# Performance work log

Hardware: AMD Instinct MI355X
Metric: run time of the kernel (lower is better)

The kernel has to match this reference:

```python
import jax, jax.numpy as jnp
import numpy as np
from jax import lax

B, L, D_MODEL = 2, 2048, 768
D_STATE, D_INNER, DT_RANK, K = 16, 1536, 48, 4


def setup_inputs() -> dict:
    key = jax.random.key(0)
    ks = jax.random.split(key, 10)
    x = jax.random.normal(ks[0], (B, L, D_MODEL), dtype=jnp.float32)
    in_proj_w = 0.02 * jax.random.normal(ks[1], (2 * D_INNER, D_MODEL), dtype=jnp.float32)
    conv_w = 0.1 * jax.random.normal(ks[2], (D_INNER, 1, K), dtype=jnp.float32)
    conv_b = 0.01 * jax.random.normal(ks[3], (D_INNER,), dtype=jnp.float32)
    # A_log initialized as log(1..d_state) per channel (as in _init_parameters)
    A_log = jnp.tile(jnp.log(jnp.arange(1, D_STATE + 1, dtype=jnp.float32)), (D_INNER, 1))
    D_param = jnp.ones((D_INNER,), dtype=jnp.float32)
    x_proj_w = 0.02 * jax.random.normal(ks[4], (DT_RANK + 2 * D_STATE, D_INNER), dtype=jnp.float32)
    dt_proj_w = jax.random.uniform(ks[5], (D_INNER, DT_RANK), minval=-0.1, maxval=0.1, dtype=jnp.float32)
    dt_proj_b = 0.01 * jax.random.normal(ks[6], (D_INNER,), dtype=jnp.float32)
    out_proj_w = 0.02 * jax.random.normal(ks[7], (D_MODEL, D_INNER), dtype=jnp.float32)
    return {"x": x, "in_proj_w": in_proj_w, "conv_w": conv_w, "conv_b": conv_b,
            "A_log": A_log, "D_param": D_param, "x_proj_w": x_proj_w,
            "dt_proj_w": dt_proj_w, "dt_proj_b": dt_proj_b, "out_proj_w": out_proj_w}


def _forward(x, in_proj_w, conv_w, conv_b, A_log, D_param, x_proj_w, dt_proj_w, dt_proj_b, out_proj_w):
    xz = jnp.einsum('bld,ed->ble', x, in_proj_w)            # [B,L,2*d_inner]
    xp, z = jnp.split(xz, 2, axis=-1)                        # [B,L,d_inner] each
    # depthwise causal conv1d: torch Conv1d(padding=3)[..., :L] == left-pad 3, valid conv
    xc = lax.conv_general_dilated(
        xp.transpose(0, 2, 1), conv_w, window_strides=(1,),
        padding=[(K - 1, 0)], feature_group_count=D_INNER)   # [B,d_inner,L]
    xc = (xc + conv_b[None, :, None]).transpose(0, 2, 1)     # [B,L,d_inner]
    xc = jax.nn.silu(xc)
    x_dbl = jnp.einsum('bld,ed->ble', xc, x_proj_w)          # [B,L,dt_rank+2*d_state]
    dt_low, Bmat, Cmat = jnp.split(x_dbl, [DT_RANK, DT_RANK + D_STATE], axis=-1)
    dt = jax.nn.softplus(jnp.einsum('blr,dr->bld', dt_low, dt_proj_w) + dt_proj_b)  # [B,L,d_inner]
    A = -jnp.exp(A_log)                                      # [d_inner,d_state]
    A_bar = jnp.exp(dt[..., None] * A[None, None])           # [B,L,d_inner,d_state]
    Bx = (dt * xc)[..., None] * Bmat[:, :, None, :]          # [B,L,d_inner,d_state]
    # time-major scan over the recurrence h = A_bar*h + B_bar*x
    A_t = A_bar.transpose(1, 0, 2, 3)
    Bx_t = Bx.transpose(1, 0, 2, 3)
    C_t = Cmat.transpose(1, 0, 2)                            # [L,B,d_state]
    h0 = jnp.zeros((B, D_INNER, D_STATE), dtype=x.dtype)

    def step(h, inp):
        a, bx, c = inp
        h = a * h + bx
        y = jnp.einsum('bds,bs->bd', h, c)
        return h, y

    _, ys = lax.scan(step, h0, (A_t, Bx_t, C_t))             # ys: [L,B,d_inner]
    y = ys.transpose(1, 0, 2)
    y = y + xc * D_param
    y = y * jax.nn.silu(z)
    return jnp.einsum('bld,md->blm', y, out_proj_w)          # [B,L,d_model]


def reference(x, in_proj_w, conv_w, conv_b, A_log, D_param, x_proj_w, dt_proj_w, dt_proj_b, out_proj_w):
    return _forward(x, in_proj_w, conv_w, conv_b, A_log, D_param, x_proj_w, dt_proj_w, dt_proj_b, out_proj_w)
```

## Files before the change

kernel.cpp:

```cpp
#include <hip/hip_runtime.h>
#include <stdint.h>

#define B_SZ    2
#define L_SEQ   2048
#define DMODEL  768
#define DSTATE  16
#define DINNER  1536
#define DTRANK  48
#define M_ROWS  4096
#define NCHUNK  32
#define TCHUNK  64
#define PADL    68

typedef __attribute__((ext_vector_type(8))) short bf16x8;
typedef __attribute__((ext_vector_type(4))) float f32x4;
typedef __attribute__((ext_vector_type(4))) unsigned int u32x4;

__device__ __forceinline__ unsigned short f2bf(float f) {
  unsigned int u = __float_as_uint(f);
  u += 0x7FFFu + ((u >> 16) & 1u);
  return (unsigned short)(u >> 16);
}
__device__ __forceinline__ float bf2f(unsigned short h) {
  return __uint_as_float(((unsigned int)h) << 16);
}
__device__ __forceinline__ float fexp(float x) {
  return __builtin_amdgcn_exp2f(x * 1.44269504088896340736f);
}
__device__ __forceinline__ float sigm(float x) {
  return 1.0f / (1.0f + fexp(-x));
}

template <int CTRL>
__device__ __forceinline__ float dpp_add(float v) {
  int x = __builtin_amdgcn_update_dpp(0, __float_as_int(v), CTRL, 0xF, 0xF, true);
  return v + __int_as_float(x);
}
__device__ __forceinline__ float row16_sum(float v) {
  v = dpp_add<0xB1>(v);
  v = dpp_add<0x4E>(v);
  v = dpp_add<0x124>(v);
  v = dpp_add<0x128>(v);
  return v;
}

__global__ void cast_all_kernel(const float* __restrict__ x, const float* __restrict__ w1,
                                const float* __restrict__ w2, const float* __restrict__ w3,
                                const float* __restrict__ dtw,
                                unsigned short* __restrict__ xbf, unsigned short* __restrict__ w1bf,
                                unsigned short* __restrict__ w2bf, unsigned short* __restrict__ w3bf,
                                unsigned short* __restrict__ dtwbf) {
  int i = blockIdx.x * 256 + threadIdx.x;
  const int n_x = M_ROWS * DMODEL;
  const int n_w1 = 2 * DINNER * DMODEL;
  const int n_w3 = DMODEL * DINNER;
  const int n_w2 = 128 * DINNER;
  const int n_dtw = DINNER * 64;
  if (i < n_x)  { xbf[i] = f2bf(x[i]); return; }  i -= n_x;
  if (i < n_w1) { w1bf[i] = f2bf(w1[i]); return; } i -= n_w1;
  if (i < n_w3) { w3bf[i] = f2bf(w3[i]); return; } i -= n_w3;
  if (i < n_w2) {
    int row = i / DINNER, col = i - row * DINNER;
    w2bf[i] = (row < (DTRANK + 2 * DSTATE)) ? f2bf(w2[row * DINNER + col]) : (unsigned short)0;
    return;
  }
  i -= n_w2;
  if (i < n_dtw) {
    int row = i >> 6, col = i & 63;
    dtwbf[i] = (col < DTRANK) ? f2bf(dtw[row * DTRANK + col]) : (unsigned short)0;
  }
}

__global__ void cast_dtlow_kernel(const float* __restrict__ xdbl, unsigned short* __restrict__ out) {
  int i = blockIdx.x * 256 + threadIdx.x;
  int row = i >> 6, col = i & 63;
  out[i] = (col < DTRANK) ? f2bf(xdbl[row * 128 + col]) : (unsigned short)0;
}

template <int EPI>
__global__ __launch_bounds__(256, 2) void gemm_bt(
    const unsigned short* __restrict__ A, const unsigned short* __restrict__ Bt,
    float* __restrict__ C, int K, int ldc, const float* __restrict__ bias) {
  __shared__ unsigned short As[128 * 40];
  __shared__ unsigned short Bs[128 * 40];
  const int tid = threadIdx.x;
  const int m0 = blockIdx.x * 128;
  const int n0 = blockIdx.y * 128;
  const int lane = tid & 63;
  const int wave = tid >> 6;
  const int wr = (wave >> 1) * 64, wc = (wave & 1) * 64;
  const int lm = lane & 15, q = lane >> 4;
  const int r = tid >> 2, sg = (tid & 3) * 8;

  f32x4 acc[4][4] = {};

  for (int k0 = 0; k0 < K; k0 += 32) {
    u32x4 a0 = *(const u32x4*)(A + (size_t)(m0 + r) * K + k0 + sg);
    u32x4 a1 = *(const u32x4*)(A + (size_t)(m0 + r + 64) * K + k0 + sg);
    u32x4 b0 = *(const u32x4*)(Bt + (size_t)(n0 + r) * K + k0 + sg);
    u32x4 b1 = *(const u32x4*)(Bt + (size_t)(n0 + r + 64) * K + k0 + sg);
    __syncthreads();
    *(u32x4*)&As[r * 40 + sg] = a0;
    *(u32x4*)&As[(r + 64) * 40 + sg] = a1;
    *(u32x4*)&Bs[r * 40 + sg] = b0;
    *(u32x4*)&Bs[(r + 64) * 40 + sg] = b1;
    __syncthreads();
    bf16x8 af[4], bq[4];
#pragma unroll
    for (int mt = 0; mt < 4; mt++)
      af[mt] = *(const bf16x8*)&As[(wr + mt * 16 + lm) * 40 + q * 8];
#pragma unroll
    for (int nt = 0; nt < 4; nt++)
      bq[nt] = *(const bf16x8*)&Bs[(wc + nt * 16 + lm) * 40 + q * 8];
#pragma unroll
    for (int mt = 0; mt < 4; mt++)
#pragma unroll
      for (int nt = 0; nt < 4; nt++)
        acc[mt][nt] = __builtin_amdgcn_mfma_f32_16x16x32_bf16(af[mt], bq[nt], acc[mt][nt], 0, 0, 0);
  }

#pragma unroll
  for (int mt = 0; mt < 4; mt++) {
    int row0 = m0 + wr + mt * 16 + q * 4;
#pragma unroll
    for (int nt = 0; nt < 4; nt++) {
      int col = n0 + wc + nt * 16 + lm;
      float bs = 0.f;
      if (EPI == 1) bs = bias[col];
#pragma unroll
      for (int i = 0; i < 4; i++) {
        float v = acc[mt][nt][i];
        if (EPI == 1) {
          v += bs;
          v = (v > 15.f) ? v : log1pf(fexp(v));
        }
        C[(size_t)(row0 + i) * ldc + col] = v;
      }
    }
  }
}

__global__ void conv_silu_kernel(const float* __restrict__ xz, const float* __restrict__ cw,
                                 const float* __restrict__ cb, unsigned short* __restrict__ xcbf) {
  int idx = blockIdx.x * 256 + threadIdx.x;
  if (idx >= B_SZ * L_SEQ * DINNER) return;
  int d = idx % DINNER;
  int bl = idx / DINNER;
  int l = bl & (L_SEQ - 1);
  float acc = cb[d];
#pragma unroll
  for (int k = 0; k < 4; k++) {
    int ll = l - 3 + k;
    if (ll >= 0) acc += cw[d * 4 + k] * xz[(size_t)(bl - 3 + k) * 3072 + d];
  }
  xcbf[idx] = f2bf(acc * sigm(acc));
}

__global__ __launch_bounds__(256) void scan_phase1(
    const float* __restrict__ dt, const unsigned short* __restrict__ xcbf,
    const float* __restrict__ xdbl, const float* __restrict__ A_log,
    float* __restrict__ P, float* __restrict__ HL) {
  __shared__ float dts[16 * PADL], xcs[16 * PADL], Bsh[16 * PADL];
  const int tid = threadIdx.x;
  const int db = blockIdx.x * 16;
  const int b = blockIdx.y;
  const int c = blockIdx.z;
  const int l0c = c * TCHUNK;
  {
    const int di = tid & 15, lg = tid >> 4;
    f32x4 dv, xv, bv;
#pragma unroll
    for (int j = 0; j < 4; j++) {
      size_t row = (size_t)(b * L_SEQ + l0c + lg * 4 + j);
      dv[j] = dt[row * DINNER + db + di];
      xv[j] = bf2f(xcbf[row * DINNER + db + di]);
      bv[j] = xdbl[row * 128 + DTRANK + di];
    }
    *(f32x4*)&dts[di * PADL + lg * 4] = dv;
    *(f32x4*)&xcs[di * PADL + lg * 4] = xv;
    *(f32x4*)&Bsh[di * PADL + lg * 4] = bv;
  }
  __syncthreads();
  const int s = tid & 15, dl = tid >> 4;
  const int d = db + dl;
  const float a2 = -fexp(A_log[d * 16 + s]) * 1.44269504f;
  float h = 0.f, sdt = 0.f;
  for (int l0 = 0; l0 < TCHUNK; l0 += 4) {
    f32x4 dtv = *(const f32x4*)&dts[dl * PADL + l0];
    f32x4 xcv = *(const f32x4*)&xcs[dl * PADL + l0];
    f32x4 Bv  = *(const f32x4*)&Bsh[s * PADL + l0];
#pragma unroll
    for (int j = 0; j < 4; j++) {
      float a = __builtin_amdgcn_exp2f(dtv[j] * a2);
      h = a * h + dtv[j] * xcv[j] * Bv[j];
      sdt += dtv[j];
    }
  }
  size_t o = ((size_t)(c * B_SZ + b) * DINNER + d) * 16 + s;
  P[o] = __builtin_amdgcn_exp2f(a2 * sdt);
  HL[o] = h;
}

__global__ void scan_phase2(const float* __restrict__ P, const float* __restrict__ HL,
                            float* __restrict__ HIN) {
  int tg = blockIdx.x * 256 + threadIdx.x;
  int s = tg & 15;
  int rem = tg >> 4;
  int d = rem % DINNER;
  int b = rem / DINNER;
  float h = 0.f;
  for (int c = 0; c < NCHUNK; c++) {
    size_t o = ((size_t)(c * B_SZ + b) * DINNER + d) * 16 + s;
    HIN[o] = h;
    h = P[o] * h + HL[o];
  }
}

__global__ __launch_bounds__(256) void scan_phase3(
    const float* __restrict__ dt, const unsigned short* __restrict__ xcbf,
    const float* __restrict__ xdbl, const float* __restrict__ A_log,
    const float* __restrict__ HIN, const float* __restrict__ xz,
    const float* __restrict__ Dp, unsigned short* __restrict__ ybf) {
  __shared__ float dts[16 * PADL], xcs[16 * PADL], Bsh[16 * PADL], Csh[16 * PADL], ysh[16 * PADL];
  const int tid = threadIdx.x;
  const int db = blockIdx.x * 16;
  const int b = blockIdx.y;
  const int c = blockIdx.z;
  const int l0c = c * TCHUNK;
  const int di = tid & 15, lg = tid >> 4;
  {
    f32x4 dv, xv, bv, cv;
#pragma unroll
    for (int j = 0; j < 4; j++) {
      size_t row = (size_t)(b * L_SEQ + l0c + lg * 4 + j);
      dv[j] = dt[row * DINNER + db + di];
      xv[j] = bf2f(xcbf[row * DINNER + db + di]);
      bv[j] = xdbl[row * 128 + DTRANK + di];
      cv[j] = xdbl[row * 128 + DTRANK + DSTATE + di];
    }
    *(f32x4*)&dts[di * PADL + lg * 4] = dv;
    *(f32x4*)&xcs[di * PADL + lg * 4] = xv;
    *(f32x4*)&Bsh[di * PADL + lg * 4] = bv;
    *(f32x4*)&Csh[di * PADL + lg * 4] = cv;
  }
  __syncthreads();
  const int s = tid & 15, dl = tid >> 4;
  const int d = db + dl;
  const float a2 = -fexp(A_log[d * 16 + s]) * 1.44269504f;
  float h = HIN[((size_t)(c * B_SZ + b) * DINNER + d) * 16 + s];
  for (int l0 = 0; l0 < TCHUNK; l0 += 4) {
    f32x4 dtv = *(const f32x4*)&dts[dl * PADL + l0];
    f32x4 xcv = *(const f32x4*)&xcs[dl * PADL + l0];
    f32x4 Bv  = *(const f32x4*)&Bsh[s * PADL + l0];
    f32x4 Cv  = *(const f32x4*)&Csh[s * PADL + l0];
    f32x4 y4;
#pragma unroll
    for (int j = 0; j < 4; j++) {
      float a = __builtin_amdgcn_exp2f(dtv[j] * a2);
      h = a * h + dtv[j] * xcv[j] * Bv[j];
      y4[j] = row16_sum(h * Cv[j]);
    }
    if (s == 0) *(f32x4*)&ysh[dl * PADL + l0] = y4;
  }
  __syncthreads();
#pragma unroll
  for (int i = 0; i < 4; i++) {
    int l = lg + i * 16;
    size_t row = (size_t)(b * L_SEQ + l0c + l);
    int gd = db + di;
    float zv = xz[row * 3072 + DINNER + gd];
    float yv = ysh[di * PADL + l] + xcs[di * PADL + l] * Dp[gd];
    ybf[row * DINNER + gd] = f2bf(yv * zv * sigm(zv));
  }
}

extern "C" void kernel_launch(void* const* d_in, const int* in_sizes, int n_in,
                              void* d_out, int out_size, void* d_ws, size_t ws_size,
                              hipStream_t stream) {
  const float* x    = (const float*)d_in[0];
  const float* w1   = (const float*)d_in[1];
  const float* cw   = (const float*)d_in[2];
  const float* cb   = (const float*)d_in[3];
  const float* alog = (const float*)d_in[4];
  const float* Dp   = (const float*)d_in[5];
  const float* w2   = (const float*)d_in[6];
  const float* dtw  = (const float*)d_in[7];
  const float* dtb  = (const float*)d_in[8];
  const float* w3   = (const float*)d_in[9];
  float* out = (float*)d_out;
  char* ws = (char*)d_ws;

  size_t off = 0;
  auto alloc = [&](size_t bytes) { size_t o = off; off += (bytes + 255) & ~(size_t)255; return o; };
  float*          xz    = (float*)(ws + alloc((size_t)M_ROWS * 3072 * 4));
  float*          xdbl  = (float*)(ws + alloc((size_t)M_ROWS * 128 * 4));
  float*          dtf   = (float*)(ws + alloc((size_t)M_ROWS * DINNER * 4));
  unsigned short* xbf   = (unsigned short*)(ws + alloc((size_t)M_ROWS * DMODEL * 2));
  unsigned short* w1bf  = (unsigned short*)(ws + alloc((size_t)2 * DINNER * DMODEL * 2));
  unsigned short* w2bf  = (unsigned short*)(ws + alloc((size_t)128 * DINNER * 2));
  unsigned short* w3bf  = (unsigned short*)(ws + alloc((size_t)DMODEL * DINNER * 2));
  unsigned short* dtlbf = (unsigned short*)(ws + alloc((size_t)M_ROWS * 64 * 2));
  unsigned short* dtwbf = (unsigned short*)(ws + alloc((size_t)DINNER * 64 * 2));
  unsigned short* xcbf  = (unsigned short*)(ws + alloc((size_t)M_ROWS * DINNER * 2));
  unsigned short* ybf   = (unsigned short*)(ws + alloc((size_t)M_ROWS * DINNER * 2));
  float*          Pbuf  = (float*)(ws + alloc((size_t)NCHUNK * B_SZ * DINNER * 16 * 4));
  float*          HLbuf = (float*)(ws + alloc((size_t)NCHUNK * B_SZ * DINNER * 16 * 4));
  float*          HINb  = (float*)(ws + alloc((size_t)NCHUNK * B_SZ * DINNER * 16 * 4));

  cast_all_kernel<<<27264, 256, 0, stream>>>(x, w1, w2, w3, dtw, xbf, w1bf, w2bf, w3bf, dtwbf);
  gemm_bt<0><<<dim3(32, 24), 256, 0, stream>>>(xbf, w1bf, xz, DMODEL, 3072, nullptr);
  conv_silu_kernel<<<24576, 256, 0, stream>>>(xz, cw, cb, xcbf);
  gemm_bt<0><<<dim3(32, 1), 256, 0, stream>>>(xcbf, w2bf, xdbl, DINNER, 128, nullptr);
  cast_dtlow_kernel<<<1024, 256, 0, stream>>>(xdbl, dtlbf);
  gemm_bt<1><<<dim3(32, 12), 256, 0, stream>>>(dtlbf, dtwbf, dtf, 64, DINNER, dtb);
  scan_phase1<<<dim3(96, 2, 32), 256, 0, stream>>>(dtf, xcbf, xdbl, alog, Pbuf, HLbuf);
  scan_phase2<<<192, 256, 0, stream>>>(Pbuf, HLbuf, HINb);
  scan_phase3<<<dim3(96, 2, 32), 256, 0, stream>>>(dtf, xcbf, xdbl, alog, HINb, xz, Dp, ybf);
  gemm_bt<0><<<dim3(32, 6), 256, 0, stream>>>(ybf, w3bf, out, DINNER, 768, nullptr);
}
```

Baseline: 337.3 us.

## Replace chunked three-phase scan with single-pass scan over transposed channel-major inputs

```diff
diff --git a/kernel.cpp b/kernel.cpp
--- a/kernel.cpp
+++ b/kernel.cpp
@@ -9,12 +9,11 @@
 #define DTRANK  48
 #define M_ROWS  4096
 #define NCHUNK  32
-#define TCHUNK  64
-#define PADL    68
 
 typedef __attribute__((ext_vector_type(8))) short bf16x8;
 typedef __attribute__((ext_vector_type(4))) float f32x4;
 typedef __attribute__((ext_vector_type(4))) unsigned int u32x4;
+typedef __attribute__((ext_vector_type(2))) unsigned int u32x2;
 
 __device__ __forceinline__ unsigned short f2bf(float f) {
   unsigned int u = __float_as_uint(f);
@@ -36,11 +35,9 @@
   int x = __builtin_amdgcn_update_dpp(0, __float_as_int(v), CTRL, 0xF, 0xF, true);
   return v + __int_as_float(x);
 }
-__device__ __forceinline__ float row16_sum(float v) {
+__device__ __forceinline__ float quad_sum(float v) {
   v = dpp_add<0xB1>(v);
   v = dpp_add<0x4E>(v);
-  v = dpp_add<0x124>(v);
-  v = dpp_add<0x128>(v);
   return v;
 }
 
@@ -122,16 +119,19 @@
 #pragma unroll
   for (int mt = 0; mt < 4; mt++) {
     int row0 = m0 + wr + mt * 16 + q * 4;
+    float bs4[4];
+    if (EPI == 2) {
+#pragma unroll
+      for (int i = 0; i < 4; i++) bs4[i] = bias[row0 + i];
+    }
 #pragma unroll
     for (int nt = 0; nt < 4; nt++) {
       int col = n0 + wc + nt * 16 + lm;
-      float bs = 0.f;
-      if (EPI == 1) bs = bias[col];
 #pragma unroll
       for (int i = 0; i < 4; i++) {
         float v = acc[mt][nt][i];
-        if (EPI == 1) {
-          v += bs;
+        if (EPI == 2) {
+          v += bs4[i];
           v = (v > 15.f) ? v : log1pf(fexp(v));
         }
         C[(size_t)(row0 + i) * ldc + col] = v;
@@ -156,121 +156,173 @@
   xcbf[idx] = f2bf(acc * sigm(acc));
 }
 
-__global__ __launch_bounds__(256) void scan_phase1(
-    const float* __restrict__ dt, const unsigned short* __restrict__ xcbf,
-    const float* __restrict__ xdbl, const float* __restrict__ A_log,
-    float* __restrict__ P, float* __restrict__ HL) {
-  __shared__ float dts[16 * PADL], xcs[16 * PADL], Bsh[16 * PADL];
+__global__ __launch_bounds__(256) void transpose_bf16(const unsigned short* __restrict__ in,
+                                                      unsigned short* __restrict__ out) {
+  __shared__ unsigned short tl[64 * 80];
+  const int r0 = blockIdx.x * 64;
+  const int c0 = blockIdx.y * 64;
   const int tid = threadIdx.x;
-  const int db = blockIdx.x * 16;
+#pragma unroll
+  for (int it = 0; it < 2; it++) {
+    int idx = tid + it * 256;
+    int rr = idx >> 3, cs = idx & 7;
+    u32x4 v = *(const u32x4*)(in + (size_t)(r0 + rr) * DINNER + c0 + cs * 8);
+    *(u32x4*)&tl[rr * 80 + cs * 8] = v;
+  }
+  __syncthreads();
+#pragma unroll
+  for (int it = 0; it < 2; it++) {
+    int idx = tid + it * 256;
+    int cc = idx & 63, rs = idx >> 6;
+    rs += it * 0;
+    rs = (tid + it * 256) >> 6;
+    unsigned int w[4];
+#pragma unroll
+    for (int p = 0; p < 4; p++) {
+      unsigned int lo = tl[(rs * 8 + 2 * p) * 80 + cc];
+      unsigned int hi = tl[(rs * 8 + 2 * p + 1) * 80 + cc];
+      w[p] = lo | (hi << 16);
+    }
+    *(u32x4*)(out + (size_t)(c0 + cc) * M_ROWS + r0 + rs * 8) = *(u32x4*)w;
+  }
+}
+
+__global__ __launch_bounds__(256) void transpose_silu(const float* __restrict__ xz,
+                                                      unsigned short* __restrict__ out) {
+  __shared__ float tl[64 * 68];
+  const int r0 = blockIdx.x * 64;
+  const int c0 = blockIdx.y * 64;
+  const int tid = threadIdx.x;
+#pragma unroll
+  for (int it = 0; it < 4; it++) {
+    int idx = tid + it * 256;
+    int rr = idx >> 4, cs = idx & 15;
+    f32x4 v = *(const f32x4*)(xz + (size_t)(r0 + rr) * 3072 + DINNER + c0 + cs * 4);
+#pragma unroll
+    for (int p = 0; p < 4; p++) v[p] = v[p] * sigm(v[p]);
+    *(f32x4*)&tl[rr * 68 + cs * 4] = v;
+  }
+  __syncthreads();
+#pragma unroll
+  for (int it = 0; it < 2; it++) {
+    int idx = tid + it * 256;
+    int cc = idx & 63, rs = idx >> 6;
+    unsigned int w[4];
+#pragma unroll
+    for (int p = 0; p < 4; p++) {
+      unsigned int lo = f2bf(tl[(rs * 8 + 2 * p) * 68 + cc]);
+      unsigned int hi = f2bf(tl[(rs * 8 + 2 * p + 1) * 68 + cc]);
+      w[p] = lo | (hi << 16);
+    }
+    *(u32x4*)(out + (size_t)(c0 + cc) * M_ROWS + r0 + rs * 8) = *(u32x4*)w;
+  }
+}
+
+__global__ void bct_kernel(const float* __restrict__ xdbl, float* __restrict__ BCt) {
+  int t = blockIdx.x * 256 + threadIdx.x;
+  int l4 = t & 511;
+  int j  = (t >> 9) & 31;
+  int b  = (t >> 14) & 1;
+  f32x4 o;
+#pragma unroll
+  for (int i = 0; i < 4; i++)
+    o[i] = xdbl[((size_t)b * L_SEQ + l4 * 4 + i) * 128 + DTRANK + j];
+  *(f32x4*)(BCt + ((size_t)b * 32 + j) * L_SEQ + l4 * 4) = o;
+}
+
+__global__ __launch_bounds__(64) void scan_single(
+    const float* __restrict__ dtT, const unsigned short* __restrict__ xcT,
+    const float* __restrict__ BCt, const unsigned short* __restrict__ szT,
+    const float* __restrict__ A_log, const float* __restrict__ Dp,
+    unsigned short* __restrict__ ybf) {
+  __shared__ float ysh[16 * 68];
+  const int lane = threadIdx.x;
+  const int s = lane & 15, dl = lane >> 4;
+  const int d = blockIdx.x * 4 + dl;
   const int b = blockIdx.y;
-  const int c = blockIdx.z;
-  const int l0c = c * TCHUNK;
-  {
-    const int di = tid & 15, lg = tid >> 4;
-    f32x4 dv, xv, bv;
-#pragma unroll
-    for (int j = 0; j < 4; j++) {
-      size_t row = (size_t)(b * L_SEQ + l0c + lg * 4 + j);
-      dv[j] = dt[row * DINNER + db + di];
-      xv[j] = bf2f(xcbf[row * DINNER + db + di]);
-      bv[j] = xdbl[row * 128 + DTRANK + di];
-    }
-    *(f32x4*)&dts[di * PADL + lg * 4] = dv;
-    *(f32x4*)&xcs[di * PADL + lg * 4] = xv;
-    *(f32x4*)&Bsh[di * PADL + lg * 4] = bv;
-  }
-  __syncthreads();
-  const int s = tid & 15, dl = tid >> 4;
-  const int d = db + dl;
+  const size_t rbase = (size_t)b * L_SEQ;
   const float a2 = -fexp(A_log[d * 16 + s]) * 1.44269504f;
-  float h = 0.f, sdt = 0.f;
-  for (int l0 = 0; l0 < TCHUNK; l0 += 4) {
-    f32x4 dtv = *(const f32x4*)&dts[dl * PADL + l0];
-    f32x4 xcv = *(const f32x4*)&xcs[dl * PADL + l0];
-    f32x4 Bv  = *(const f32x4*)&Bsh[s * PADL + l0];
-#pragma unroll
-    for (int j = 0; j < 4; j++) {
-      float a = __builtin_amdgcn_exp2f(dtv[j] * a2);
-      h = a * h + dtv[j] * xcv[j] * Bv[j];
-      sdt += dtv[j];
-    }
-  }
-  size_t o = ((size_t)(c * B_SZ + b) * DINNER + d) * 16 + s;
-  P[o] = __builtin_amdgcn_exp2f(a2 * sdt);
-  HL[o] = h;
-}
-
-__global__ void scan_phase2(const float* __restrict__ P, const float* __restrict__ HL,
-                            float* __restrict__ HIN) {
-  int tg = blockIdx.x * 256 + threadIdx.x;
-  int s = tg & 15;
-  int rem = tg >> 4;
-  int d = rem % DINNER;
-  int b = rem / DINNER;
+  const float dpv = Dp[d];
+  const float* dtrow = dtT + (size_t)d * M_ROWS + rbase;
+  const unsigned short* xcrow = xcT + (size_t)d * M_ROWS + rbase;
+  const unsigned short* szrow = szT + (size_t)d * M_ROWS + rbase;
+  const float* Brow = BCt + ((size_t)b * 32 + s) * L_SEQ;
+  const float* Crow = BCt + ((size_t)b * 32 + 16 + s) * L_SEQ;
+  float* ywp = &ysh[(dl * 4 + (s >> 2)) * 68 + (s & 3)];
+  const bool sb0 = (s & 1) != 0, sb1 = (s & 2) != 0;
   float h = 0.f;
+
+  f32x4 ndt0 = *(const f32x4*)(dtrow);
+  f32x4 ndt1 = *(const f32x4*)(dtrow + 4);
+  u32x4 nxc  = *(const u32x4*)(xcrow);
+  f32x4 nB0  = *(const f32x4*)(Brow);
+  f32x4 nB1  = *(const f32x4*)(Brow + 4);
+  f32x4 nC0  = *(const f32x4*)(Crow);
+  f32x4 nC1  = *(const f32x4*)(Crow + 4);
+
   for (int c = 0; c < NCHUNK; c++) {
-    size_t o = ((size_t)(c * B_SZ + b) * DINNER + d) * 16 + s;
-    HIN[o] = h;
-    h = P[o] * h + HL[o];
-  }
-}
-
-__global__ __launch_bounds__(256) void scan_phase3(
-    const float* __restrict__ dt, const unsigned short* __restrict__ xcbf,
-    const float* __restrict__ xdbl, const float* __restrict__ A_log,
-    const float* __restrict__ HIN, const float* __restrict__ xz,
-    const float* __restrict__ Dp, unsigned short* __restrict__ ybf) {
-  __shared__ float dts[16 * PADL], xcs[16 * PADL], Bsh[16 * PADL], Csh[16 * PADL], ysh[16 * PADL];
-  const int tid = threadIdx.x;
-  const int db = blockIdx.x * 16;
-  const int b = blockIdx.y;
-  const int c = blockIdx.z;
-  const int l0c = c * TCHUNK;
-  const int di = tid & 15, lg = tid >> 4;
-  {
-    f32x4 dv, xv, bv, cv;
-#pragma unroll
-    for (int j = 0; j < 4; j++) {
-      size_t row = (size_t)(b * L_SEQ + l0c + lg * 4 + j);
-      dv[j] = dt[row * DINNER + db + di];
-      xv[j] = bf2f(xcbf[row * DINNER + db + di]);
-      bv[j] = xdbl[row * 128 + DTRANK + di];
-      cv[j] = xdbl[row * 128 + DTRANK + DSTATE + di];
-    }
-    *(f32x4*)&dts[di * PADL + lg * 4] = dv;
-    *(f32x4*)&xcs[di * PADL + lg * 4] = xv;
-    *(f32x4*)&Bsh[di * PADL + lg * 4] = bv;
-    *(f32x4*)&Csh[di * PADL + lg * 4] = cv;
-  }
-  __syncthreads();
-  const int s = tid & 15, dl = tid >> 4;
-  const int d = db + dl;
-  const float a2 = -fexp(A_log[d * 16 + s]) * 1.44269504f;
-  float h = HIN[((size_t)(c * B_SZ + b) * DINNER + d) * 16 + s];
-  for (int l0 = 0; l0 < TCHUNK; l0 += 4) {
-    f32x4 dtv = *(const f32x4*)&dts[dl * PADL + l0];
-    f32x4 xcv = *(const f32x4*)&xcs[dl * PADL + l0];
-    f32x4 Bv  = *(const f32x4*)&Bsh[s * PADL + l0];
-    f32x4 Cv  = *(const f32x4*)&Csh[s * PADL + l0];
-    f32x4 y4;
-#pragma unroll
-    for (int j = 0; j < 4; j++) {
-      float a = __builtin_amdgcn_exp2f(dtv[j] * a2);
-      h = a * h + dtv[j] * xcv[j] * Bv[j];
-      y4[j] = row16_sum(h * Cv[j]);
-    }
-    if (s == 0) *(f32x4*)&ysh[dl * PADL + l0] = y4;
-  }
-  __syncthreads();
-#pragma unroll
-  for (int i = 0; i < 4; i++) {
-    int l = lg + i * 16;
-    size_t row = (size_t)(b * L_SEQ + l0c + l);
-    int gd = db + di;
-    float zv = xz[row * 3072 + DINNER + gd];
-    float yv = ysh[di * PADL + l] + xcs[di * PADL + l] * Dp[gd];
-    ybf[row * DINNER + gd] = f2bf(yv * zv * sigm(zv));
+#pragma unroll 1
+    for (int g = 0; g < 8; g++) {
+      f32x4 dt0 = ndt0, dt1 = ndt1, B0 = nB0, B1 = nB1, C0 = nC0, C1 = nC1;
+      u32x4 xcv = nxc;
+      int ln = c * 64 + g * 8 + 8;
+      if (ln == L_SEQ) ln = 0;
+      ndt0 = *(const f32x4*)(dtrow + ln);
+      ndt1 = *(const f32x4*)(dtrow + ln + 4);
+      nxc  = *(const u32x4*)(xcrow + ln);
+      nB0  = *(const f32x4*)(Brow + ln);
+      nB1  = *(const f32x4*)(Brow + ln + 4);
+      nC0  = *(const f32x4*)(Crow + ln);
+      nC1  = *(const f32x4*)(Crow + ln + 4);
+
+      float xf[8];
+#pragma unroll
+      for (int jp = 0; jp < 4; jp++) {
+        unsigned int w = xcv[jp];
+        xf[2 * jp]     = __uint_as_float(w << 16);
+        xf[2 * jp + 1] = __uint_as_float(w & 0xFFFF0000u);
+      }
+      float p[8];
+#pragma unroll
+      for (int j = 0; j < 8; j++) {
+        float dtj = (j < 4) ? dt0[j] : dt1[j - 4];
+        float Bj  = (j < 4) ? B0[j]  : B1[j - 4];
+        float Cj  = (j < 4) ? C0[j]  : C1[j - 4];
+        float a = __builtin_amdgcn_exp2f(dtj * a2);
+        h = a * h + dtj * xf[j] * Bj;
+        p[j] = h * Cj;
+      }
+#pragma unroll
+      for (int half = 0; half < 2; half++) {
+        float q0 = quad_sum(p[half * 4 + 0]);
+        float q1 = quad_sum(p[half * 4 + 1]);
+        float q2 = quad_sum(p[half * 4 + 2]);
+        float q3 = quad_sum(p[half * 4 + 3]);
+        float v01 = sb0 ? q1 : q0;
+        float v23 = sb0 ? q3 : q2;
+        ywp[g * 8 + half * 4] = sb1 ? v23 : v01;
+      }
+    }
+    {
+      f32x4 y0 = *(const f32x4*)&ysh[(dl * 4 + 0) * 68 + s * 4];
+      f32x4 y1 = *(const f32x4*)&ysh[(dl * 4 + 1) * 68 + s * 4];
+      f32x4 y2 = *(const f32x4*)&ysh[(dl * 4 + 2) * 68 + s * 4];
+      f32x4 y3 = *(const f32x4*)&ysh[(dl * 4 + 3) * 68 + s * 4];
+      f32x4 ys = y0 + y1 + y2 + y3;
+      const int le = c * 64 + s * 4;
+      u32x2 xcu = *(const u32x2*)(xcrow + le);
+      u32x2 szu = *(const u32x2*)(szrow + le);
+      float xcf[4] = {__uint_as_float(xcu[0] << 16), __uint_as_float(xcu[0] & 0xFFFF0000u),
+                      __uint_as_float(xcu[1] << 16), __uint_as_float(xcu[1] & 0xFFFF0000u)};
+      float szf[4] = {__uint_as_float(szu[0] << 16), __uint_as_float(szu[0] & 0xFFFF0000u),
+                      __uint_as_float(szu[1] << 16), __uint_as_float(szu[1] & 0xFFFF0000u)};
+      size_t rr0 = rbase + le;
+#pragma unroll
+      for (int i = 0; i < 4; i++) {
+        float yv = ys[i] + xcf[i] * dpv;
+        ybf[(rr0 + i) * DINNER + d] = f2bf(yv * szf[i]);
+      }
+    }
   }
 }
 
@@ -292,9 +344,11 @@
 
   size_t off = 0;
   auto alloc = [&](size_t bytes) { size_t o = off; off += (bytes + 255) & ~(size_t)255; return o; };
-  float*          xz    = (float*)(ws + alloc((size_t)M_ROWS * 3072 * 4));
+  char*           xzr   = ws + alloc((size_t)M_ROWS * 3072 * 4);
+  float*          xz    = (float*)xzr;
+  float*          dtT   = (float*)xzr;
+  unsigned short* ybf   = (unsigned short*)(xzr + (size_t)DINNER * M_ROWS * 4);
   float*          xdbl  = (float*)(ws + alloc((size_t)M_ROWS * 128 * 4));
-  float*          dtf   = (float*)(ws + alloc((size_t)M_ROWS * DINNER * 4));
   unsigned short* xbf   = (unsigned short*)(ws + alloc((size_t)M_ROWS * DMODEL * 2));
   unsigned short* w1bf  = (unsigned short*)(ws + alloc((size_t)2 * DINNER * DMODEL * 2));
   unsigned short* w2bf  = (unsigned short*)(ws + alloc((size_t)128 * DINNER * 2));
@@ -302,19 +356,19 @@
   unsigned short* dtlbf = (unsigned short*)(ws + alloc((size_t)M_ROWS * 64 * 2));
   unsigned short* dtwbf = (unsigned short*)(ws + alloc((size_t)DINNER * 64 * 2));
   unsigned short* xcbf  = (unsigned short*)(ws + alloc((size_t)M_ROWS * DINNER * 2));
-  unsigned short* ybf   = (unsigned short*)(ws + alloc((size_t)M_ROWS * DINNER * 2));
-  float*          Pbuf  = (float*)(ws + alloc((size_t)NCHUNK * B_SZ * DINNER * 16 * 4));
-  float*          HLbuf = (float*)(ws + alloc((size_t)NCHUNK * B_SZ * DINNER * 16 * 4));
-  float*          HINb  = (float*)(ws + alloc((size_t)NCHUNK * B_SZ * DINNER * 16 * 4));
+  unsigned short* xcT   = (unsigned short*)(ws + alloc((size_t)DINNER * M_ROWS * 2));
+  unsigned short* szbf  = (unsigned short*)(ws + alloc((size_t)DINNER * M_ROWS * 2));
+  float*          BCt   = (float*)(ws + alloc((size_t)B_SZ * 32 * L_SEQ * 4));
 
   cast_all_kernel<<<27264, 256, 0, stream>>>(x, w1, w2, w3, dtw, xbf, w1bf, w2bf, w3bf, dtwbf);
   gemm_bt<0><<<dim3(32, 24), 256, 0, stream>>>(xbf, w1bf, xz, DMODEL, 3072, nullptr);
   conv_silu_kernel<<<24576, 256, 0, stream>>>(xz, cw, cb, xcbf);
+  transpose_silu<<<dim3(64, 24), 256, 0, stream>>>(xz, szbf);
+  transpose_bf16<<<dim3(64, 24), 256, 0, stream>>>(xcbf, xcT);
   gemm_bt<0><<<dim3(32, 1), 256, 0, stream>>>(xcbf, w2bf, xdbl, DINNER, 128, nullptr);
+  bct_kernel<<<128, 256, 0, stream>>>(xdbl, BCt);
   cast_dtlow_kernel<<<1024, 256, 0, stream>>>(xdbl, dtlbf);
-  gemm_bt<1><<<dim3(32, 12), 256, 0, stream>>>(dtlbf, dtwbf, dtf, 64, DINNER, dtb);
-  scan_phase1<<<dim3(96, 2, 32), 256, 0, stream>>>(dtf, xcbf, xdbl, alog, Pbuf, HLbuf);
-  scan_phase2<<<192, 256, 0, stream>>>(Pbuf, HLbuf, HINb);
-  scan_phase3<<<dim3(96, 2, 32), 256, 0, stream>>>(dtf, xcbf, xdbl, alog, HINb, xz, Dp, ybf);
+  gemm_bt<2><<<dim3(12, 32), 256, 0, stream>>>(dtwbf, dtlbf, dtT, 64, M_ROWS, dtb);
+  scan_single<<<dim3(384, 2), 64, 0, stream>>>(dtT, xcT, BCt, szbf, alog, Dp, ybf);
   gemm_bt<0><<<dim3(32, 6), 256, 0, stream>>>(ybf, w3bf, out, DINNER, 768, nullptr);
 }
```

Result: slower. 406.9 us (+20.6%).
